# Performance work log

Hardware: AMD Instinct MI355X
Metric: run time of the kernel (lower is better)

Reference implementation:

```python
import jax, jax.numpy as jnp
import numpy as np
import math

B, S, D = 8, 2048, 512
WINDOW = 30

def setup_inputs() -> dict:
    key = jax.random.key(0)
    ks = jax.random.split(key, 9)
    s = 1.0 / math.sqrt(D)
    return {
        "hidden_states": jax.random.normal(ks[0], (B, S, D), jnp.float32),
        "Wq": jax.random.normal(ks[1], (D, D), jnp.float32) * s,
        "bq": jax.random.normal(ks[2], (D,), jnp.float32) * s,
        "Wk": jax.random.normal(ks[3], (D, D), jnp.float32) * s,
        "bk": jax.random.normal(ks[4], (D,), jnp.float32) * s,
        "Wv": jax.random.normal(ks[5], (D, D), jnp.float32) * s,
        "bv": jax.random.normal(ks[6], (D,), jnp.float32) * s,
        "Wg": jax.random.normal(ks[7], (D, 1), jnp.float32) * s,
        "bg": jax.random.normal(ks[8], (1,), jnp.float32) * s,
    }

def reference(hidden_states, Wq, bq, Wk, bk, Wv, bv, Wg, bg):
    seq_len = hidden_states.shape[1]
    scale = math.sqrt(hidden_states.shape[-1])
    Q = hidden_states @ Wq + bq
    K = hidden_states @ Wk + bk
    V = hidden_states @ Wv + bv
    # [B, S, S] dense scores, single head
    scores = jnp.einsum('bsd,btd->bst', Q, K) / scale
    global_out = jnp.einsum('bst,btd->bsd', jax.nn.softmax(scores, axis=-1), V)
    pos = jnp.arange(seq_len)
    window_mask = jnp.abs(pos[:, None] - pos[None, :]) <= WINDOW  # [S, S]
    local_scores = scores + jnp.where(window_mask, 0.0, -1e9)
    local_out = jnp.einsum('bst,btd->bsd', jax.nn.softmax(local_scores, axis=-1), V)
    gate = jax.nn.sigmoid(hidden_states @ Wg + bg)  # [B, S, 1]
    return (1.0 - gate) * global_out + gate * local_out
```

## Files before the change

### kernel.cpp

```cpp
#include <hip/hip_runtime.h>
#include <math.h>

#define B_N   8
#define S_LEN 2048
#define D_DIM 512
#define M_TOT (B_N * S_LEN)
#define WIN   30

typedef short bf16x8 __attribute__((ext_vector_type(8)));
typedef float f32x4  __attribute__((ext_vector_type(4)));
typedef unsigned short u16;
typedef unsigned int   u32;

__device__ __forceinline__ u16 f2bf(float f) {
    union { float f; u32 u; } v; v.f = f;
    u32 r = v.u + 0x7fffu + ((v.u >> 16) & 1u);
    return (u16)(r >> 16);
}
__device__ __forceinline__ float bf2f(u16 u) {
    union { u32 u; float f; } v; v.u = ((u32)u) << 16; return v.f;
}

__device__ __forceinline__ void gl2lds(const u16* g, u16* l) {
    __builtin_amdgcn_global_load_lds((const __attribute__((address_space(1))) void*)g,
                                     (__attribute__((address_space(3))) void*)l,
                                     16, 0, 0);
}

__device__ __forceinline__ int xcd_logical() {
    const int n = gridDim.x;
    const int hb = blockIdx.x;
    return (hb & 7) * (n >> 3) + (hb >> 3);
}

#define VM_WAIT(N) asm volatile("s_waitcnt vmcnt(" #N ")" ::: "memory")
#define BAR() do { __builtin_amdgcn_s_barrier(); asm volatile("" ::: "memory"); } while (0)

__global__ __launch_bounds__(256)
void convert_gate(const float* __restrict__ X, const float* __restrict__ Wg,
                  const float* __restrict__ bg, u16* __restrict__ Xb, float* __restrict__ gate) {
    int wv = threadIdx.x >> 6, lane = threadIdx.x & 63;
    int row = blockIdx.x * 4 + wv;
    const float4* x4 = (const float4*)(X + (size_t)row * D_DIM);
    const float4* w4 = (const float4*)Wg;
    float acc = 0.f;
    ushort4 o0, o1;
    {
        float4 a = x4[lane * 2], w = w4[lane * 2];
        acc += a.x * w.x + a.y * w.y + a.z * w.z + a.w * w.w;
        o0.x = f2bf(a.x); o0.y = f2bf(a.y); o0.z = f2bf(a.z); o0.w = f2bf(a.w);
        float4 b = x4[lane * 2 + 1], v = w4[lane * 2 + 1];
        acc += b.x * v.x + b.y * v.y + b.z * v.z + b.w * v.w;
        o1.x = f2bf(b.x); o1.y = f2bf(b.y); o1.z = f2bf(b.z); o1.w = f2bf(b.w);
    }
    ushort4* xb4 = (ushort4*)(Xb + (size_t)row * D_DIM);
    xb4[lane * 2] = o0;
    xb4[lane * 2 + 1] = o1;
#pragma unroll
    for (int o = 32; o; o >>= 1) acc += __shfl_xor(acc, o);
    if (lane == 0) gate[row] = 1.f / (1.f + __expf(-(acc + bg[0])));
}

__global__ __launch_bounds__(256) void transpose_w3(const float* __restrict__ Wq, const float* __restrict__ Wk,
                                                    const float* __restrict__ Wv, u16* __restrict__ Wt3) {
    const float* W = blockIdx.z == 0 ? Wq : (blockIdx.z == 1 ? Wk : Wv);
    u16* Wt = Wt3 + (size_t)blockIdx.z * D_DIM * D_DIM;
    __shared__ float t[32][33];
    int k0 = blockIdx.x * 32, n0 = blockIdx.y * 32;
    int tx = threadIdx.x & 31, ty = threadIdx.x >> 5;
#pragma unroll
    for (int r = ty; r < 32; r += 8) t[r][tx] = W[(size_t)(k0 + r) * D_DIM + n0 + tx];
    __syncthreads();
#pragma unroll
    for (int r = ty; r < 32; r += 8) Wt[(size_t)(n0 + r) * D_DIM + k0 + tx] = f2bf(t[tx][r]);
}

__global__ __launch_bounds__(256) void pack_bias(const float* __restrict__ bq, const float* __restrict__ bk,
                                                 const float* __restrict__ bv, float* __restrict__ b3) {
    int i = blockIdx.x * 256 + threadIdx.x;
    b3[i] = bq[i]; b3[512 + i] = bk[i]; b3[1024 + i] = bv[i];
}

template<int EPI>
__global__ __launch_bounds__(512, 2)
void gemm256(const u16* __restrict__ A, const u16* __restrict__ Bt,
             int lda, int ldb, int K, int nx, int ny,
             const float* __restrict__ aux, void* __restrict__ Cv, int ldc, float scale,
             long long zA, long long zB, long long zC, long long zAux) {
    const int logical = xcd_logical();
    const int x = logical % nx;
    const int t2 = logical / nx;
    const int y = t2 % ny;
    const int z = t2 / ny;

    A   += zA * z;
    Bt  += zB * z;
    if (aux) aux += zAux * z;

    constexpr int BUF = 16384;
    __shared__ u16 smem[3 * BUF];
    const int tid  = threadIdx.x;
    const int lane = tid & 63;
    const int wave = tid >> 6;
    const int wr = wave >> 2, wc = wave & 3;
    const int m0 = y * 256, n0 = x * 256;

    f32x4 acc[8][4];
#pragma unroll
    for (int i = 0; i < 8; i++)
#pragma unroll
        for (int j = 0; j < 4; j++) acc[i][j] = (f32x4){0.f, 0.f, 0.f, 0.f};

    auto stageA = [&](int b, int k0) {
#pragma unroll
        for (int j = 0; j < 2; j++) {
            int c = j * 512 + tid;
            int r = c >> 2;
            int s = ((c & 3) ^ ((c >> 3) & 3)) << 3;
            gl2lds(A + (size_t)(m0 + r) * lda + (k0 + s),
                   smem + b * BUF + j * 4096 + wave * 512);
        }
    };
    auto stageB = [&](int b, int k0) {
#pragma unroll
        for (int j = 0; j < 2; j++) {
            int c = j * 512 + tid;
            int r = c >> 2;
            int s = ((c & 3) ^ ((c >> 3) & 3)) << 3;
            gl2lds(Bt + (size_t)(n0 + r) * ldb + (k0 + s),
                   smem + b * BUF + 8192 + j * 4096 + wave * 512);
        }
    };

    const int nt = K >> 5;
    stageA(0, 0); stageB(0, 0); stageA(1, 32); stageB(1, 32);

    const int ks = lane >> 4;
    for (int t = 0; t < nt; ++t) {
        const u16* bA = smem + (t % 3) * BUF;
        const u16* bB = bA + 8192;
        if (t == nt - 1) { VM_WAIT(0); } else { VM_WAIT(4); }
        BAR();
        if (t + 2 < nt) stageA((t + 2) % 3, (t + 2) << 5);
        bf16x8 bfr[4], af[4];
#pragma unroll
        for (int n = 0; n < 4; n++) {
            int r = wc * 64 + n * 16 + (lane & 15);
            bfr[n] = *(const bf16x8*)&bB[r * 32 + (ks ^ ((r >> 1) & 3)) * 8];
        }
#pragma unroll
        for (int m = 0; m < 4; m++) {
            int r = wr * 128 + m * 16 + (lane & 15);
            af[m] = *(const bf16x8*)&bA[r * 32 + (ks ^ ((r >> 1) & 3)) * 8];
        }
        __builtin_amdgcn_s_setprio(1);
#pragma unroll
        for (int m = 0; m < 4; m++)
#pragma unroll
            for (int n = 0; n < 4; n++)
                acc[m][n] = __builtin_amdgcn_mfma_f32_16x16x32_bf16(af[m], bfr[n], acc[m][n], 0, 0, 0);
        __builtin_amdgcn_s_setprio(0);
        BAR();
        if (t + 2 < nt) stageB((t + 2) % 3, (t + 2) << 5);
#pragma unroll
        for (int m = 0; m < 4; m++) {
            int r = wr * 128 + (m + 4) * 16 + (lane & 15);
            af[m] = *(const bf16x8*)&bA[r * 32 + (ks ^ ((r >> 1) & 3)) * 8];
        }
        __builtin_amdgcn_s_setprio(1);
#pragma unroll
        for (int m = 0; m < 4; m++)
#pragma unroll
            for (int n = 0; n < 4; n++)
                acc[m + 4][n] = __builtin_amdgcn_mfma_f32_16x16x32_bf16(af[m], bfr[n], acc[m + 4][n], 0, 0, 0);
        __builtin_amdgcn_s_setprio(0);
    }

    u16* Cb = (u16*)Cv + zC * z;
#pragma unroll
    for (int m = 0; m < 8; m++) {
        int rbase = m0 + wr * 128 + m * 16 + ((lane >> 4) << 2);
#pragma unroll
        for (int n = 0; n < 4; n++) {
            int col = n0 + wc * 64 + n * 16 + (lane & 15);
#pragma unroll
            for (int rg = 0; rg < 4; rg++) {
                int row = rbase + rg;
                float v = acc[m][n][rg];
                if (EPI == 0) {
                    Cb[(size_t)row * ldc + col] = f2bf(v + aux[col]);
                } else {
                    Cb[(size_t)row * ldc + col] = f2bf(v * scale);
                }
            }
        }
    }
}

template<int EPI>
__global__ __launch_bounds__(256, 6)
void gemm_bt(const u16* __restrict__ A, const u16* __restrict__ Bt,
             int lda, int ldb, int K, int nx, int ny,
             const float* __restrict__ aux, void* __restrict__ Cv, int ldc, float scale,
             long long zA, long long zB, long long zC, long long zAux) {
    const int logical = xcd_logical();
    const int x = logical % nx;
    const int t2 = logical / nx;
    const int y = t2 % ny;
    const int z = t2 / ny;

    A   += zA * z;
    Bt  += zB * z;
    if (aux) aux += zAux * z;

    __shared__ u16 smem[3 * 8192];
    const int tid  = threadIdx.x;
    const int lane = tid & 63;
    const int wave = tid >> 6;
    const int wr = wave >> 1, wc = wave & 1;
    const int m0 = y * 128, n0 = x * 128;

    f32x4 acc[4][4];
#pragma unroll
    for (int i = 0; i < 4; i++)
#pragma unroll
        for (int j = 0; j < 4; j++) acc[i][j] = (f32x4){0.f, 0.f, 0.f, 0.f};

    const int c0 = tid, c1 = tid + 256;
    const int r0c = c0 >> 2, k0c = (((c0 & 3) ^ ((c0 >> 3) & 3)) << 3);
    const int r1c = c1 >> 2, k1c = (((c1 & 3) ^ ((c1 >> 3) & 3)) << 3);

    auto stage = [&](int b, int k0) {
        u16* dA = smem + b * 8192 + wave * 512;
        u16* dB = smem + b * 8192 + 4096 + wave * 512;
        gl2lds(A + (size_t)(m0 + r0c) * lda + (k0 + k0c), dA);
        gl2lds(A + (size_t)(m0 + r1c) * lda + (k0 + k1c), dA + 2048);
        gl2lds(Bt + (size_t)(n0 + r0c) * ldb + (k0 + k0c), dB);
        gl2lds(Bt + (size_t)(n0 + r1c) * ldb + (k0 + k1c), dB + 2048);
    };
    auto compute = [&](int b) {
        const u16* bA = smem + b * 8192;
        const u16* bB = smem + b * 8192 + 4096;
        const int ks = lane >> 4;
        bf16x8 af[4], bfr[4];
#pragma unroll
        for (int m = 0; m < 4; m++) {
            int r = wr * 64 + m * 16 + (lane & 15);
            af[m] = *(const bf16x8*)&bA[r * 32 + (ks ^ ((r >> 1) & 3)) * 8];
        }
#pragma unroll
        for (int n = 0; n < 4; n++) {
            int r = wc * 64 + n * 16 + (lane & 15);
            bfr[n] = *(const bf16x8*)&bB[r * 32 + (ks ^ ((r >> 1) & 3)) * 8];
        }
#pragma unroll
        for (int m = 0; m < 4; m++)
#pragma unroll
            for (int n = 0; n < 4; n++)
                acc[m][n] = __builtin_amdgcn_mfma_f32_16x16x32_bf16(af[m], bfr[n], acc[m][n], 0, 0, 0);
    };

    const int nt = K >> 5;
    stage(0, 0); stage(1, 32);

    int t = 0;
    for (; t < nt - 1; ++t) {
        VM_WAIT(4);
        BAR();
        if (t + 2 < nt) stage((t + 2) % 3, (t + 2) << 5);
        compute(t % 3);
    }
    VM_WAIT(0);
    BAR();
    compute((nt - 1) % 3);

    u16*   Cb = (EPI == 1) ? ((u16*)Cv + zC * z) : nullptr;
    float* Cf = (EPI == 2) ? ((float*)Cv + zC * z) : nullptr;

#pragma unroll
    for (int m = 0; m < 4; m++) {
        int rbase = m0 + wr * 64 + m * 16 + ((lane >> 4) << 2);
#pragma unroll
        for (int n = 0; n < 4; n++) {
            int col = n0 + wc * 64 + n * 16 + (lane & 15);
#pragma unroll
            for (int rg = 0; rg < 4; rg++) {
                int row = rbase + rg;
                float v = acc[m][n][rg];
                if (EPI == 1) {
                    Cb[(size_t)row * ldc + col] = f2bf(v + aux[row]);
                } else {
                    Cf[(size_t)row * ldc + col] = v * scale;
                }
            }
        }
    }
}

__global__ __launch_bounds__(256)
void softmax_fuse(u16* __restrict__ sc, const float* __restrict__ gate) {
    const int logical = xcd_logical();
    const int i = logical & (S_LEN - 1);
    const int z = logical >> 11;
    const int tid = threadIdx.x;
    const int wv = tid >> 6, lane = tid & 63;
    sc   += (size_t)z * S_LEN * S_LEN;
    gate += (size_t)z * S_LEN;

    __shared__ float r0[4], r1[4], mll[2];

    u16* scrow = sc + (size_t)i * S_LEN;
    uint4 raw = ((const uint4*)scrow)[tid];

    int jlo = i - WIN; if (jlo < 0) jlo = 0;
    int jhi = i + WIN; if (jhi > S_LEN - 1) jhi = S_LEN - 1;
    int cnt = jhi - jlo + 1;
    float bvv = (tid < cnt) ? bf2f(scrow[jlo + tid]) : -3.0e38f;
    float g = gate[i];

    float sv[8];
    sv[0] = bf2f((u16)(raw.x & 0xffff)); sv[1] = bf2f((u16)(raw.x >> 16));
    sv[2] = bf2f((u16)(raw.y & 0xffff)); sv[3] = bf2f((u16)(raw.y >> 16));
    sv[4] = bf2f((u16)(raw.z & 0xffff)); sv[5] = bf2f((u16)(raw.z >> 16));
    sv[6] = bf2f((u16)(raw.w & 0xffff)); sv[7] = bf2f((u16)(raw.w >> 16));

    float mx = fmaxf(fmaxf(fmaxf(sv[0], sv[1]), fmaxf(sv[2], sv[3])),
                     fmaxf(fmaxf(sv[4], sv[5]), fmaxf(sv[6], sv[7])));
#pragma unroll
    for (int o = 32; o; o >>= 1) mx = fmaxf(mx, __shfl_xor(mx, o));
    if (lane == 0) r0[wv] = mx;
    __syncthreads();
    float mg = fmaxf(fmaxf(r0[0], r0[1]), fmaxf(r0[2], r0[3]));

    float ev[8];
#pragma unroll
    for (int k = 0; k < 8; k++) ev[k] = __expf(sv[k] - mg);
    float se = ev[0] + ev[1] + ev[2] + ev[3] + ev[4] + ev[5] + ev[6] + ev[7];
#pragma unroll
    for (int o = 32; o; o >>= 1) se += __shfl_xor(se, o);
    if (lane == 0) r1[wv] = se;

    if (wv == 0) {
        float ml = bvv;
#pragma unroll
        for (int o = 32; o; o >>= 1) ml = fmaxf(ml, __shfl_xor(ml, o));
        float e = (lane < cnt) ? __expf(bvv - ml) : 0.f;
        float s2 = e;
#pragma unroll
        for (int o = 32; o; o >>= 1) s2 += __shfl_xor(s2, o);
        if (lane == 0) { mll[0] = ml; mll[1] = 1.f / s2; }
    }
    __syncthreads();
    float invl = (1.f - g) / (r1[0] + r1[1] + r1[2] + r1[3]);
    float ml  = mll[0];
    float ill = g * mll[1];

    const int c0 = tid * 8;
    u32 pk_[4];
#pragma unroll
    for (int h = 0; h < 4; h++) {
        float rA = ev[2 * h] * invl;
        float rB = ev[2 * h + 1] * invl;
        int colA = c0 + 2 * h;
        if ((u32)(colA - i + WIN) <= 2u * WIN)     rA += __expf(sv[2 * h] - ml) * ill;
        if ((u32)(colA + 1 - i + WIN) <= 2u * WIN) rB += __expf(sv[2 * h + 1] - ml) * ill;
        pk_[h] = (u32)f2bf(rA) | ((u32)f2bf(rB) << 16);
    }
    uint4 pw = {pk_[0], pk_[1], pk_[2], pk_[3]};
    ((uint4*)scrow)[tid] = pw;
}

extern "C" void kernel_launch(void* const* d_in, const int* in_sizes, int n_in,
                              void* d_out, int out_size, void* d_ws, size_t ws_size,
                              hipStream_t stream) {
    const float* X  = (const float*)d_in[0];
    const float* Wq = (const float*)d_in[1];
    const float* bq = (const float*)d_in[2];
    const float* Wk = (const float*)d_in[3];
    const float* bk = (const float*)d_in[4];
    const float* Wv = (const float*)d_in[5];
    const float* bv = (const float*)d_in[6];
    const float* Wg = (const float*)d_in[7];
    const float* bg = (const float*)d_in[8];
    float* out = (float*)d_out;

    char* p = (char*)d_ws;
    u16* Xb    = (u16*)p;  p += (size_t)M_TOT * D_DIM * 2;
    u16* Wt3   = (u16*)p;  p += (size_t)3 * D_DIM * D_DIM * 2;
    u16* QKV   = (u16*)p;  p += (size_t)2 * M_TOT * D_DIM * 2;
    u16* Vt    = (u16*)p;  p += (size_t)M_TOT * D_DIM * 2;
    float* gate  = (float*)p; p += (size_t)M_TOT * 4;
    float* bias3 = (float*)p; p += (size_t)3 * D_DIM * 4;
    u16* scores = (u16*)p;
    size_t base_used = (size_t)(p - (char*)d_ws);
    size_t per_batch = (size_t)S_LEN * S_LEN * 2;
    int nbuf = (int)((ws_size - base_used) / per_batch);
    if (nbuf > B_N) nbuf = B_N;
    if (nbuf < 1) nbuf = 1;

    u16* Qb = QKV;
    u16* Kb = QKV + (size_t)M_TOT * D_DIM;

    convert_gate<<<dim3(M_TOT / 4), 256, 0, stream>>>(X, Wg, bg, Xb, gate);
    transpose_w3<<<dim3(16, 16, 3), 256, 0, stream>>>(Wq, Wk, Wv, Wt3);
    pack_bias<<<dim3(2), 256, 0, stream>>>(bq, bk, bv, bias3);

    gemm256<0><<<dim3(2 * 64 * 2), 512, 0, stream>>>(
        Xb, Wt3, 512, 512, 512, 2, 64, bias3, QKV, 512, 1.f,
        0LL, (long long)D_DIM * D_DIM, (long long)M_TOT * D_DIM, (long long)D_DIM);

    gemm_bt<1><<<dim3(128 * 4), 256, 0, stream>>>(
        Wt3 + (size_t)2 * D_DIM * D_DIM, Xb, 512, 512, 512, 128, 4, bv, Vt, M_TOT, 1.f,
        0LL, 0LL, 0LL, 0LL);

    const float sc = 1.0f / sqrtf((float)D_DIM);
    for (int g0 = 0; g0 < B_N; g0 += nbuf) {
        int gcnt = B_N - g0 < nbuf ? B_N - g0 : nbuf;
        gemm256<3><<<dim3(8 * 8 * gcnt), 512, 0, stream>>>(
            Qb + (size_t)g0 * S_LEN * D_DIM, Kb + (size_t)g0 * S_LEN * D_DIM,
            512, 512, 512, 8, 8, nullptr, scores, S_LEN, sc,
            (long long)S_LEN * D_DIM, (long long)S_LEN * D_DIM,
            (long long)S_LEN * S_LEN, 0LL);
        softmax_fuse<<<dim3(S_LEN * gcnt), 256, 0, stream>>>(
            scores, gate + (size_t)g0 * S_LEN);
        gemm_bt<2><<<dim3(4 * 16 * gcnt), 256, 0, stream>>>(
            scores, Vt + (size_t)g0 * S_LEN,
            S_LEN, M_TOT, S_LEN, 4, 16, nullptr,
            out + (size_t)g0 * S_LEN * D_DIM, 512, 1.f,
            (long long)S_LEN * S_LEN, (long long)S_LEN,
            (long long)S_LEN * D_DIM, 0LL);
    }
}
```

Measured before the change: 174.6 us.

## Fuse softmax into score GEMM epilogue and PV GEMM prologue

Removes the separate row-softmax pass over the score matrix. The QK^T GEMM epilogue now accumulates per-row exp sums and band (window) exp sums through atomics. A small kernel folds these with the gate into per-row coefficients, and the PV GEMM recomputes exp(score) times those coefficients while staging A tiles into LDS. This saves a full read and write of the B×S×S bf16 score tensor. The cost is exps with no max subtraction, which can overflow for large scores, plus atomics and extra ALU work in the PV GEMM's load path.

```diff
diff --git a/kernel.cpp b/kernel.cpp
--- a/kernel.cpp
+++ b/kernel.cpp
@@ -34,6 +34,7 @@
 }
 
 #define VM_WAIT(N) asm volatile("s_waitcnt vmcnt(" #N ")" ::: "memory")
+#define LGKM0()    asm volatile("s_waitcnt lgkmcnt(0)" ::: "memory")
 #define BAR() do { __builtin_amdgcn_s_barrier(); asm volatile("" ::: "memory"); } while (0)
 
 __global__ __launch_bounds__(256)
@@ -81,11 +82,21 @@
     b3[i] = bq[i]; b3[512 + i] = bk[i]; b3[1024 + i] = bv[i];
 }
 
+__global__ __launch_bounds__(256)
+void coef_combine(const float* __restrict__ rs, const float* __restrict__ bs,
+                  const float* __restrict__ gate, float2* __restrict__ coef) {
+    int i = blockIdx.x * 256 + threadIdx.x;
+    float g = gate[i];
+    float2 c; c.x = (1.f - g) / rs[i]; c.y = g / bs[i];
+    coef[i] = c;
+}
+
 template<int EPI>
 __global__ __launch_bounds__(512, 2)
 void gemm256(const u16* __restrict__ A, const u16* __restrict__ Bt,
              int lda, int ldb, int K, int nx, int ny,
              const float* __restrict__ aux, void* __restrict__ Cv, int ldc, float scale,
+             float* __restrict__ rowsum, float* __restrict__ bandsum,
              long long zA, long long zB, long long zC, long long zAux) {
     const int logical = xcd_logical();
     const int x = logical % nx;
@@ -96,6 +107,7 @@
     A   += zA * z;
     Bt  += zB * z;
     if (aux) aux += zAux * z;
+    if (EPI == 3) { rowsum += 2048LL * z; bandsum += 2048LL * z; }
 
     constexpr int BUF = 16384;
     __shared__ u16 smem[3 * BUF];
@@ -104,6 +116,7 @@
     const int wave = tid >> 6;
     const int wr = wave >> 2, wc = wave & 3;
     const int m0 = y * 256, n0 = x * 256;
+    const int l15 = lane & 15;
 
     f32x4 acc[8][4];
 #pragma unroll
@@ -145,12 +158,12 @@
         bf16x8 bfr[4], af[4];
 #pragma unroll
         for (int n = 0; n < 4; n++) {
-            int r = wc * 64 + n * 16 + (lane & 15);
+            int r = wc * 64 + n * 16 + l15;
             bfr[n] = *(const bf16x8*)&bB[r * 32 + (ks ^ ((r >> 1) & 3)) * 8];
         }
 #pragma unroll
         for (int m = 0; m < 4; m++) {
-            int r = wr * 128 + m * 16 + (lane & 15);
+            int r = wr * 128 + m * 16 + l15;
             af[m] = *(const bf16x8*)&bA[r * 32 + (ks ^ ((r >> 1) & 3)) * 8];
         }
         __builtin_amdgcn_s_setprio(1);
@@ -164,7 +177,7 @@
         if (t + 2 < nt) stageB((t + 2) % 3, (t + 2) << 5);
 #pragma unroll
         for (int m = 0; m < 4; m++) {
-            int r = wr * 128 + (m + 4) * 16 + (lane & 15);
+            int r = wr * 128 + (m + 4) * 16 + l15;
             af[m] = *(const bf16x8*)&bA[r * 32 + (ks ^ ((r >> 1) & 3)) * 8];
         }
         __builtin_amdgcn_s_setprio(1);
@@ -174,15 +187,20 @@
             for (int n = 0; n < 4; n++)
                 acc[m + 4][n] = __builtin_amdgcn_mfma_f32_16x16x32_bf16(af[m], bfr[n], acc[m + 4][n], 0, 0, 0);
         __builtin_amdgcn_s_setprio(0);
+        BAR();
     }
 
     u16* Cb = (u16*)Cv + zC * z;
+    const bool diag = (EPI == 3) && (x - y <= 1) && (y - x <= 1);
+
 #pragma unroll
     for (int m = 0; m < 8; m++) {
         int rbase = m0 + wr * 128 + m * 16 + ((lane >> 4) << 2);
+        float se[4] = {0.f, 0.f, 0.f, 0.f};
+        float sb[4] = {0.f, 0.f, 0.f, 0.f};
 #pragma unroll
         for (int n = 0; n < 4; n++) {
-            int col = n0 + wc * 64 + n * 16 + (lane & 15);
+            int col = n0 + wc * 64 + n * 16 + l15;
 #pragma unroll
             for (int rg = 0; rg < 4; rg++) {
                 int row = rbase + rg;
@@ -190,28 +208,42 @@
                 if (EPI == 0) {
                     Cb[(size_t)row * ldc + col] = f2bf(v + aux[col]);
                 } else {
-                    Cb[(size_t)row * ldc + col] = f2bf(v * scale);
+                    u16 h = f2bf(v * scale);
+                    Cb[(size_t)row * ldc + col] = h;
+                    float e = __expf(bf2f(h));
+                    se[rg] += e;
+                    if (diag) {
+                        int d = col - row;
+                        if (d * d <= WIN * WIN) sb[rg] += e;
+                    }
                 }
             }
         }
-    }
-}
-
-template<int EPI>
+        if (EPI == 3) {
+#pragma unroll
+            for (int rg = 0; rg < 4; rg++) {
+                float s1 = se[rg];
+                s1 += __shfl_xor(s1, 1); s1 += __shfl_xor(s1, 2);
+                s1 += __shfl_xor(s1, 4); s1 += __shfl_xor(s1, 8);
+                if (l15 == 0) atomicAdd(&rowsum[rbase + rg - m0 + m0], s1);
+                if (diag) {
+                    float s2 = sb[rg];
+                    s2 += __shfl_xor(s2, 1); s2 += __shfl_xor(s2, 2);
+                    s2 += __shfl_xor(s2, 4); s2 += __shfl_xor(s2, 8);
+                    if (l15 == 0) atomicAdd(&bandsum[rbase + rg], s2);
+                }
+            }
+        }
+    }
+}
+
 __global__ __launch_bounds__(256, 6)
-void gemm_bt(const u16* __restrict__ A, const u16* __restrict__ Bt,
-             int lda, int ldb, int K, int nx, int ny,
-             const float* __restrict__ aux, void* __restrict__ Cv, int ldc, float scale,
-             long long zA, long long zB, long long zC, long long zAux) {
+void gemm_bt1(const u16* __restrict__ A, const u16* __restrict__ Bt,
+              int lda, int ldb, int K, int nx, int ny,
+              const float* __restrict__ aux, u16* __restrict__ C, int ldc) {
     const int logical = xcd_logical();
     const int x = logical % nx;
-    const int t2 = logical / nx;
-    const int y = t2 % ny;
-    const int z = t2 / ny;
-
-    A   += zA * z;
-    Bt  += zB * z;
-    if (aux) aux += zAux * z;
+    const int y = (logical / nx) % ny;
 
     __shared__ u16 smem[3 * 8192];
     const int tid  = threadIdx.x;
@@ -262,7 +294,6 @@
 
     const int nt = K >> 5;
     stage(0, 0); stage(1, 32);
-
     int t = 0;
     for (; t < nt - 1; ++t) {
         VM_WAIT(4);
@@ -274,9 +305,6 @@
     BAR();
     compute((nt - 1) % 3);
 
-    u16*   Cb = (EPI == 1) ? ((u16*)Cv + zC * z) : nullptr;
-    float* Cf = (EPI == 2) ? ((float*)Cv + zC * z) : nullptr;
-
 #pragma unroll
     for (int m = 0; m < 4; m++) {
         int rbase = m0 + wr * 64 + m * 16 + ((lane >> 4) << 2);
@@ -286,88 +314,151 @@
 #pragma unroll
             for (int rg = 0; rg < 4; rg++) {
                 int row = rbase + rg;
-                float v = acc[m][n][rg];
-                if (EPI == 1) {
-                    Cb[(size_t)row * ldc + col] = f2bf(v + aux[row]);
-                } else {
-                    Cf[(size_t)row * ldc + col] = v * scale;
-                }
+                C[(size_t)row * ldc + col] = f2bf(acc[m][n][rg] + aux[row]);
             }
         }
     }
 }
 
-__global__ __launch_bounds__(256)
-void softmax_fuse(u16* __restrict__ sc, const float* __restrict__ gate) {
+__global__ __launch_bounds__(256, 4)
+void gemm_pv(const u16* __restrict__ S, const u16* __restrict__ Bt,
+             const float2* __restrict__ coef, float* __restrict__ out,
+             int lda, int ldb, int K, int nx, int ny,
+             long long zA, long long zB, long long zC) {
     const int logical = xcd_logical();
-    const int i = logical & (S_LEN - 1);
-    const int z = logical >> 11;
-    const int tid = threadIdx.x;
-    const int wv = tid >> 6, lane = tid & 63;
-    sc   += (size_t)z * S_LEN * S_LEN;
-    gate += (size_t)z * S_LEN;
-
-    __shared__ float r0[4], r1[4], mll[2];
-
-    u16* scrow = sc + (size_t)i * S_LEN;
-    uint4 raw = ((const uint4*)scrow)[tid];
-
-    int jlo = i - WIN; if (jlo < 0) jlo = 0;
-    int jhi = i + WIN; if (jhi > S_LEN - 1) jhi = S_LEN - 1;
-    int cnt = jhi - jlo + 1;
-    float bvv = (tid < cnt) ? bf2f(scrow[jlo + tid]) : -3.0e38f;
-    float g = gate[i];
-
-    float sv[8];
-    sv[0] = bf2f((u16)(raw.x & 0xffff)); sv[1] = bf2f((u16)(raw.x >> 16));
-    sv[2] = bf2f((u16)(raw.y & 0xffff)); sv[3] = bf2f((u16)(raw.y >> 16));
-    sv[4] = bf2f((u16)(raw.z & 0xffff)); sv[5] = bf2f((u16)(raw.z >> 16));
-    sv[6] = bf2f((u16)(raw.w & 0xffff)); sv[7] = bf2f((u16)(raw.w >> 16));
-
-    float mx = fmaxf(fmaxf(fmaxf(sv[0], sv[1]), fmaxf(sv[2], sv[3])),
-                     fmaxf(fmaxf(sv[4], sv[5]), fmaxf(sv[6], sv[7])));
-#pragma unroll
-    for (int o = 32; o; o >>= 1) mx = fmaxf(mx, __shfl_xor(mx, o));
-    if (lane == 0) r0[wv] = mx;
-    __syncthreads();
-    float mg = fmaxf(fmaxf(r0[0], r0[1]), fmaxf(r0[2], r0[3]));
-
-    float ev[8];
-#pragma unroll
-    for (int k = 0; k < 8; k++) ev[k] = __expf(sv[k] - mg);
-    float se = ev[0] + ev[1] + ev[2] + ev[3] + ev[4] + ev[5] + ev[6] + ev[7];
-#pragma unroll
-    for (int o = 32; o; o >>= 1) se += __shfl_xor(se, o);
-    if (lane == 0) r1[wv] = se;
-
-    if (wv == 0) {
-        float ml = bvv;
-#pragma unroll
-        for (int o = 32; o; o >>= 1) ml = fmaxf(ml, __shfl_xor(ml, o));
-        float e = (lane < cnt) ? __expf(bvv - ml) : 0.f;
-        float s2 = e;
-#pragma unroll
-        for (int o = 32; o; o >>= 1) s2 += __shfl_xor(s2, o);
-        if (lane == 0) { mll[0] = ml; mll[1] = 1.f / s2; }
-    }
-    __syncthreads();
-    float invl = (1.f - g) / (r1[0] + r1[1] + r1[2] + r1[3]);
-    float ml  = mll[0];
-    float ill = g * mll[1];
-
-    const int c0 = tid * 8;
-    u32 pk_[4];
-#pragma unroll
-    for (int h = 0; h < 4; h++) {
-        float rA = ev[2 * h] * invl;
-        float rB = ev[2 * h + 1] * invl;
-        int colA = c0 + 2 * h;
-        if ((u32)(colA - i + WIN) <= 2u * WIN)     rA += __expf(sv[2 * h] - ml) * ill;
-        if ((u32)(colA + 1 - i + WIN) <= 2u * WIN) rB += __expf(sv[2 * h + 1] - ml) * ill;
-        pk_[h] = (u32)f2bf(rA) | ((u32)f2bf(rB) << 16);
-    }
-    uint4 pw = {pk_[0], pk_[1], pk_[2], pk_[3]};
-    ((uint4*)scrow)[tid] = pw;
+    const int x = logical % nx;
+    const int t2 = logical / nx;
+    const int y = t2 % ny;
+    const int z = t2 / ny;
+
+    S    += zA * z;
+    Bt   += zB * z;
+    coef += 2048LL * z;
+    float* outz = out + zC * z;
+
+    __shared__ u16 bufA[4096];
+    __shared__ u16 bufB[2][4096];
+    const int tid = threadIdx.x, lane = tid & 63, wave = tid >> 6;
+    const int wr = wave >> 1, wc = wave & 1;
+    const int m0 = y * 128, n0 = x * 128;
+    const int ks = lane >> 4, l15 = lane & 15;
+
+    f32x4 acc[4][4];
+#pragma unroll
+    for (int i = 0; i < 4; i++)
+#pragma unroll
+        for (int j = 0; j < 4; j++) acc[i][j] = (f32x4){0.f, 0.f, 0.f, 0.f};
+
+    const int c0 = tid, c1 = tid + 256;
+    const int r0 = c0 >> 2, k0c = (((c0 & 3) ^ ((c0 >> 3) & 3)) << 3);
+    const int r1 = c1 >> 2, k1c = (((c1 & 3) ^ ((c1 >> 3) & 3)) << 3);
+    const int arow0 = m0 + r0, arow1 = m0 + r1;
+    const float2 cf0 = coef[arow0], cf1 = coef[arow1];
+    const u16* Sr0 = S + (size_t)arow0 * lda;
+    const u16* Sr1 = S + (size_t)arow1 * lda;
+
+    auto glB = [&](int bsel, int k0) {
+        u16* dB = &bufB[bsel][wave * 512];
+        gl2lds(Bt + (size_t)(n0 + r0) * ldb + (k0 + k0c), dB);
+        gl2lds(Bt + (size_t)(n0 + r1) * ldb + (k0 + k1c), dB + 2048);
+    };
+
+    auto mkR = [&](uint4 q, float2 cf, int row, int cb) -> uint4 {
+        u32 w[4] = {q.x, q.y, q.z, q.w};
+        u32 o[4];
+#pragma unroll
+        for (int wi = 0; wi < 4; wi++) {
+            float s0 = bf2f((u16)(w[wi] & 0xffffu));
+            float s1 = bf2f((u16)(w[wi] >> 16));
+            float e0 = __expf(s0), e1 = __expf(s1);
+            int d0 = cb + 2 * wi - row, d1 = d0 + 1;
+            float r0v = cf.x * e0 + ((d0 * d0 <= WIN * WIN) ? cf.y * e0 : 0.f);
+            float r1v = cf.x * e1 + ((d1 * d1 <= WIN * WIN) ? cf.y * e1 : 0.f);
+            o[wi] = (u32)f2bf(r0v) | ((u32)f2bf(r1v) << 16);
+        }
+        uint4 r; r.x = o[0]; r.y = o[1]; r.z = o[2]; r.w = o[3];
+        return r;
+    };
+
+    auto compute = [&](int bsel) {
+        bf16x8 af[4], bfr[4];
+#pragma unroll
+        for (int m = 0; m < 4; m++) {
+            int r = wr * 64 + m * 16 + l15;
+            af[m] = *(const bf16x8*)&bufA[r * 32 + ((ks ^ ((r >> 1) & 3)) << 3)];
+        }
+#pragma unroll
+        for (int n = 0; n < 4; n++) {
+            int r = wc * 64 + n * 16 + l15;
+            bfr[n] = *(const bf16x8*)&bufB[bsel][r * 32 + ((ks ^ ((r >> 1) & 3)) << 3)];
+        }
+#pragma unroll
+        for (int m = 0; m < 4; m++)
+#pragma unroll
+            for (int n = 0; n < 4; n++)
+                acc[m][n] = __builtin_amdgcn_mfma_f32_16x16x32_bf16(af[m], bfr[n], acc[m][n], 0, 0, 0);
+    };
+
+    const int nt = K >> 5;
+    uint4 qa0, qa1, qb0, qb1;
+    qa0 = *(const uint4*)(Sr0 + k0c);
+    qa1 = *(const uint4*)(Sr1 + k1c);
+    glB(0, 0);
+
+    for (int t = 0; t < nt; t += 2) {
+        if (t + 1 < nt) {
+            int k1 = (t + 1) << 5;
+            qb0 = *(const uint4*)(Sr0 + k1 + k0c);
+            qb1 = *(const uint4*)(Sr1 + k1 + k1c);
+            glB(1, k1);
+        }
+        VM_WAIT(4);
+        {
+            int k0 = t << 5;
+            uint4 o0 = mkR(qa0, cf0, arow0, k0 + k0c);
+            uint4 o1 = mkR(qa1, cf1, arow1, k0 + k1c);
+            *(uint4*)&bufA[c0 * 8] = o0;
+            *(uint4*)&bufA[c1 * 8] = o1;
+        }
+        LGKM0();
+        BAR();
+        compute(0);
+        BAR();
+        if (t + 2 < nt) {
+            int k2 = (t + 2) << 5;
+            qa0 = *(const uint4*)(Sr0 + k2 + k0c);
+            qa1 = *(const uint4*)(Sr1 + k2 + k1c);
+            glB(0, k2);
+        }
+        if (t + 1 < nt) {
+            if (t + 1 == nt - 1) { VM_WAIT(0); } else { VM_WAIT(4); }
+            {
+                int k1 = (t + 1) << 5;
+                uint4 o0 = mkR(qb0, cf0, arow0, k1 + k0c);
+                uint4 o1 = mkR(qb1, cf1, arow1, k1 + k1c);
+                *(uint4*)&bufA[c0 * 8] = o0;
+                *(uint4*)&bufA[c1 * 8] = o1;
+            }
+            LGKM0();
+            BAR();
+            compute(1);
+            BAR();
+        }
+    }
+
+#pragma unroll
+    for (int m = 0; m < 4; m++) {
+        int rbase = m0 + wr * 64 + m * 16 + ((lane >> 4) << 2);
+#pragma unroll
+        for (int n = 0; n < 4; n++) {
+            int col = n0 + wc * 64 + n * 16 + l15;
+#pragma unroll
+            for (int rg = 0; rg < 4; rg++) {
+                int row = rbase + rg;
+                outz[(size_t)row * D_DIM + col] = acc[m][n][rg];
+            }
+        }
+    }
 }
 
 extern "C" void kernel_launch(void* const* d_in, const int* in_sizes, int n_in,
@@ -391,6 +482,9 @@
     u16* Vt    = (u16*)p;  p += (size_t)M_TOT * D_DIM * 2;
     float* gate  = (float*)p; p += (size_t)M_TOT * 4;
     float* bias3 = (float*)p; p += (size_t)3 * D_DIM * 4;
+    float* rowsum  = (float*)p; p += (size_t)M_TOT * 4;
+    float* bandsum = (float*)p; p += (size_t)M_TOT * 4;
+    float2* coef   = (float2*)p; p += (size_t)M_TOT * 8;
     u16* scores = (u16*)p;
     size_t base_used = (size_t)(p - (char*)d_ws);
     size_t per_batch = (size_t)S_LEN * S_LEN * 2;
@@ -401,17 +495,18 @@
     u16* Qb = QKV;
     u16* Kb = QKV + (size_t)M_TOT * D_DIM;
 
+    hipMemsetAsync(rowsum, 0, (size_t)M_TOT * 8, stream);
+
     convert_gate<<<dim3(M_TOT / 4), 256, 0, stream>>>(X, Wg, bg, Xb, gate);
     transpose_w3<<<dim3(16, 16, 3), 256, 0, stream>>>(Wq, Wk, Wv, Wt3);
     pack_bias<<<dim3(2), 256, 0, stream>>>(bq, bk, bv, bias3);
 
     gemm256<0><<<dim3(2 * 64 * 2), 512, 0, stream>>>(
-        Xb, Wt3, 512, 512, 512, 2, 64, bias3, QKV, 512, 1.f,
+        Xb, Wt3, 512, 512, 512, 2, 64, bias3, QKV, 512, 1.f, nullptr, nullptr,
         0LL, (long long)D_DIM * D_DIM, (long long)M_TOT * D_DIM, (long long)D_DIM);
 
-    gemm_bt<1><<<dim3(128 * 4), 256, 0, stream>>>(
-        Wt3 + (size_t)2 * D_DIM * D_DIM, Xb, 512, 512, 512, 128, 4, bv, Vt, M_TOT, 1.f,
-        0LL, 0LL, 0LL, 0LL);
+    gemm_bt1<<<dim3(128 * 4), 256, 0, stream>>>(
+        Wt3 + (size_t)2 * D_DIM * D_DIM, Xb, 512, 512, 512, 128, 4, bv, Vt, M_TOT);
 
     const float sc = 1.0f / sqrtf((float)D_DIM);
     for (int g0 = 0; g0 < B_N; g0 += nbuf) {
@@ -419,15 +514,17 @@
         gemm256<3><<<dim3(8 * 8 * gcnt), 512, 0, stream>>>(
             Qb + (size_t)g0 * S_LEN * D_DIM, Kb + (size_t)g0 * S_LEN * D_DIM,
             512, 512, 512, 8, 8, nullptr, scores, S_LEN, sc,
+            rowsum + (size_t)g0 * S_LEN, bandsum + (size_t)g0 * S_LEN,
             (long long)S_LEN * D_DIM, (long long)S_LEN * D_DIM,
             (long long)S_LEN * S_LEN, 0LL);
-        softmax_fuse<<<dim3(S_LEN * gcnt), 256, 0, stream>>>(
-            scores, gate + (size_t)g0 * S_LEN);
-        gemm_bt<2><<<dim3(4 * 16 * gcnt), 256, 0, stream>>>(
-            scores, Vt + (size_t)g0 * S_LEN,
-            S_LEN, M_TOT, S_LEN, 4, 16, nullptr,
-            out + (size_t)g0 * S_LEN * D_DIM, 512, 1.f,
+        coef_combine<<<dim3(gcnt * S_LEN / 256), 256, 0, stream>>>(
+            rowsum + (size_t)g0 * S_LEN, bandsum + (size_t)g0 * S_LEN,
+            gate + (size_t)g0 * S_LEN, coef + (size_t)g0 * S_LEN);
+        gemm_pv<<<dim3(4 * 16 * gcnt), 256, 0, stream>>>(
+            scores, Vt + (size_t)g0 * S_LEN, coef + (size_t)g0 * S_LEN,
+            out + (size_t)g0 * S_LEN * D_DIM,
+            S_LEN, M_TOT, S_LEN, 4, 16,
             (long long)S_LEN * S_LEN, (long long)S_LEN,
-            (long long)S_LEN * D_DIM, 0LL);
-    }
-}
+            (long long)S_LEN * D_DIM);
+    }
+}
```

After: 237.3 us. 1.36x slower.

## Fuse exp and row/band sums into QK^T epilogue, simplify softmax to normalize

Applied to the files above, without the earlier changes.

The score GEMM epilogue now writes exp(scaled score) without max subtraction and accumulates per-row full sums and windowed band sums via shuffle reductions and atomics. The softmax kernel becomes a single-pass normalize that scales each element by the gate-weighted reciprocal sums. This removes the max/sum reductions and the band reload from the softmax pass. In exchange it adds atomics and a memset, and drops max-subtraction, which relies on scores staying small enough not to overflow. An extra barrier is also added at the end of each GEMM k-loop iteration.

```diff
diff --git a/kernel.cpp b/kernel.cpp
--- a/kernel.cpp
+++ b/kernel.cpp
@@ -86,6 +86,7 @@
 void gemm256(const u16* __restrict__ A, const u16* __restrict__ Bt,
              int lda, int ldb, int K, int nx, int ny,
              const float* __restrict__ aux, void* __restrict__ Cv, int ldc, float scale,
+             float* __restrict__ rowsum, float* __restrict__ bandsum,
              long long zA, long long zB, long long zC, long long zAux) {
     const int logical = xcd_logical();
     const int x = logical % nx;
@@ -96,6 +97,7 @@
     A   += zA * z;
     Bt  += zB * z;
     if (aux) aux += zAux * z;
+    if (EPI == 3) { rowsum += 2048LL * z; bandsum += 2048LL * z; }
 
     constexpr int BUF = 16384;
     __shared__ u16 smem[3 * BUF];
@@ -104,6 +106,7 @@
     const int wave = tid >> 6;
     const int wr = wave >> 2, wc = wave & 3;
     const int m0 = y * 256, n0 = x * 256;
+    const int l15 = lane & 15;
 
     f32x4 acc[8][4];
 #pragma unroll
@@ -145,12 +148,12 @@
         bf16x8 bfr[4], af[4];
 #pragma unroll
         for (int n = 0; n < 4; n++) {
-            int r = wc * 64 + n * 16 + (lane & 15);
+            int r = wc * 64 + n * 16 + l15;
             bfr[n] = *(const bf16x8*)&bB[r * 32 + (ks ^ ((r >> 1) & 3)) * 8];
         }
 #pragma unroll
         for (int m = 0; m < 4; m++) {
-            int r = wr * 128 + m * 16 + (lane & 15);
+            int r = wr * 128 + m * 16 + l15;
             af[m] = *(const bf16x8*)&bA[r * 32 + (ks ^ ((r >> 1) & 3)) * 8];
         }
         __builtin_amdgcn_s_setprio(1);
@@ -164,7 +167,7 @@
         if (t + 2 < nt) stageB((t + 2) % 3, (t + 2) << 5);
 #pragma unroll
         for (int m = 0; m < 4; m++) {
-            int r = wr * 128 + (m + 4) * 16 + (lane & 15);
+            int r = wr * 128 + (m + 4) * 16 + l15;
             af[m] = *(const bf16x8*)&bA[r * 32 + (ks ^ ((r >> 1) & 3)) * 8];
         }
         __builtin_amdgcn_s_setprio(1);
@@ -174,15 +177,20 @@
             for (int n = 0; n < 4; n++)
                 acc[m + 4][n] = __builtin_amdgcn_mfma_f32_16x16x32_bf16(af[m], bfr[n], acc[m + 4][n], 0, 0, 0);
         __builtin_amdgcn_s_setprio(0);
+        BAR();
     }
 
     u16* Cb = (u16*)Cv + zC * z;
+    const bool diag = (EPI == 3) && (x - y <= 1) && (y - x <= 1);
+
 #pragma unroll
     for (int m = 0; m < 8; m++) {
         int rbase = m0 + wr * 128 + m * 16 + ((lane >> 4) << 2);
+        float se[4] = {0.f, 0.f, 0.f, 0.f};
+        float sb[4] = {0.f, 0.f, 0.f, 0.f};
 #pragma unroll
         for (int n = 0; n < 4; n++) {
-            int col = n0 + wc * 64 + n * 16 + (lane & 15);
+            int col = n0 + wc * 64 + n * 16 + l15;
 #pragma unroll
             for (int rg = 0; rg < 4; rg++) {
                 int row = rbase + rg;
@@ -190,7 +198,28 @@
                 if (EPI == 0) {
                     Cb[(size_t)row * ldc + col] = f2bf(v + aux[col]);
                 } else {
-                    Cb[(size_t)row * ldc + col] = f2bf(v * scale);
+                    float e = __expf(v * scale);
+                    Cb[(size_t)row * ldc + col] = f2bf(e);
+                    se[rg] += e;
+                    if (diag) {
+                        int d = col - row;
+                        if (d * d <= WIN * WIN) sb[rg] += e;
+                    }
+                }
+            }
+        }
+        if (EPI == 3) {
+#pragma unroll
+            for (int rg = 0; rg < 4; rg++) {
+                float s1 = se[rg];
+                s1 += __shfl_xor(s1, 1); s1 += __shfl_xor(s1, 2);
+                s1 += __shfl_xor(s1, 4); s1 += __shfl_xor(s1, 8);
+                if (l15 == 0) atomicAdd(&rowsum[rbase + rg], s1);
+                if (diag) {
+                    float s2 = sb[rg];
+                    s2 += __shfl_xor(s2, 1); s2 += __shfl_xor(s2, 2);
+                    s2 += __shfl_xor(s2, 4); s2 += __shfl_xor(s2, 8);
+                    if (l15 == 0) atomicAdd(&bandsum[rbase + rg], s2);
                 }
             }
         }
@@ -262,7 +291,6 @@
 
     const int nt = K >> 5;
     stage(0, 0); stage(1, 32);
-
     int t = 0;
     for (; t < nt - 1; ++t) {
         VM_WAIT(4);
@@ -298,76 +326,34 @@
 }
 
 __global__ __launch_bounds__(256)
-void softmax_fuse(u16* __restrict__ sc, const float* __restrict__ gate) {
+void normalize_r(u16* __restrict__ sc, const float* __restrict__ rs,
+                 const float* __restrict__ bs, const float* __restrict__ gate) {
     const int logical = xcd_logical();
     const int i = logical & (S_LEN - 1);
     const int z = logical >> 11;
     const int tid = threadIdx.x;
-    const int wv = tid >> 6, lane = tid & 63;
-    sc   += (size_t)z * S_LEN * S_LEN;
-    gate += (size_t)z * S_LEN;
-
-    __shared__ float r0[4], r1[4], mll[2];
-
-    u16* scrow = sc + (size_t)i * S_LEN;
-    uint4 raw = ((const uint4*)scrow)[tid];
-
-    int jlo = i - WIN; if (jlo < 0) jlo = 0;
-    int jhi = i + WIN; if (jhi > S_LEN - 1) jhi = S_LEN - 1;
-    int cnt = jhi - jlo + 1;
-    float bvv = (tid < cnt) ? bf2f(scrow[jlo + tid]) : -3.0e38f;
-    float g = gate[i];
-
-    float sv[8];
-    sv[0] = bf2f((u16)(raw.x & 0xffff)); sv[1] = bf2f((u16)(raw.x >> 16));
-    sv[2] = bf2f((u16)(raw.y & 0xffff)); sv[3] = bf2f((u16)(raw.y >> 16));
-    sv[4] = bf2f((u16)(raw.z & 0xffff)); sv[5] = bf2f((u16)(raw.z >> 16));
-    sv[6] = bf2f((u16)(raw.w & 0xffff)); sv[7] = bf2f((u16)(raw.w >> 16));
-
-    float mx = fmaxf(fmaxf(fmaxf(sv[0], sv[1]), fmaxf(sv[2], sv[3])),
-                     fmaxf(fmaxf(sv[4], sv[5]), fmaxf(sv[6], sv[7])));
-#pragma unroll
-    for (int o = 32; o; o >>= 1) mx = fmaxf(mx, __shfl_xor(mx, o));
-    if (lane == 0) r0[wv] = mx;
-    __syncthreads();
-    float mg = fmaxf(fmaxf(r0[0], r0[1]), fmaxf(r0[2], r0[3]));
-
-    float ev[8];
-#pragma unroll
-    for (int k = 0; k < 8; k++) ev[k] = __expf(sv[k] - mg);
-    float se = ev[0] + ev[1] + ev[2] + ev[3] + ev[4] + ev[5] + ev[6] + ev[7];
-#pragma unroll
-    for (int o = 32; o; o >>= 1) se += __shfl_xor(se, o);
-    if (lane == 0) r1[wv] = se;
-
-    if (wv == 0) {
-        float ml = bvv;
-#pragma unroll
-        for (int o = 32; o; o >>= 1) ml = fmaxf(ml, __shfl_xor(ml, o));
-        float e = (lane < cnt) ? __expf(bvv - ml) : 0.f;
-        float s2 = e;
-#pragma unroll
-        for (int o = 32; o; o >>= 1) s2 += __shfl_xor(s2, o);
-        if (lane == 0) { mll[0] = ml; mll[1] = 1.f / s2; }
-    }
-    __syncthreads();
-    float invl = (1.f - g) / (r1[0] + r1[1] + r1[2] + r1[3]);
-    float ml  = mll[0];
-    float ill = g * mll[1];
-
+    sc += (size_t)z * S_LEN * S_LEN;
+
+    const int ri = z * S_LEN + i;
+    float g  = gate[ri];
+    float cx = (1.f - g) / rs[ri];
+    float cy = g / bs[ri];
+
+    u16* row = sc + (size_t)i * S_LEN;
+    uint4 q = ((const uint4*)row)[tid];
+    u32 w[4] = {q.x, q.y, q.z, q.w};
     const int c0 = tid * 8;
-    u32 pk_[4];
 #pragma unroll
     for (int h = 0; h < 4; h++) {
-        float rA = ev[2 * h] * invl;
-        float rB = ev[2 * h + 1] * invl;
-        int colA = c0 + 2 * h;
-        if ((u32)(colA - i + WIN) <= 2u * WIN)     rA += __expf(sv[2 * h] - ml) * ill;
-        if ((u32)(colA + 1 - i + WIN) <= 2u * WIN) rB += __expf(sv[2 * h + 1] - ml) * ill;
-        pk_[h] = (u32)f2bf(rA) | ((u32)f2bf(rB) << 16);
-    }
-    uint4 pw = {pk_[0], pk_[1], pk_[2], pk_[3]};
-    ((uint4*)scrow)[tid] = pw;
+        float e0 = bf2f((u16)(w[h] & 0xffffu));
+        float e1 = bf2f((u16)(w[h] >> 16));
+        int d0 = c0 + 2 * h - i, d1 = d0 + 1;
+        float r0 = e0 * (cx + ((d0 * d0 <= WIN * WIN) ? cy : 0.f));
+        float r1 = e1 * (cx + ((d1 * d1 <= WIN * WIN) ? cy : 0.f));
+        w[h] = (u32)f2bf(r0) | ((u32)f2bf(r1) << 16);
+    }
+    uint4 o; o.x = w[0]; o.y = w[1]; o.z = w[2]; o.w = w[3];
+    ((uint4*)row)[tid] = o;
 }
 
 extern "C" void kernel_launch(void* const* d_in, const int* in_sizes, int n_in,
@@ -391,6 +377,8 @@
     u16* Vt    = (u16*)p;  p += (size_t)M_TOT * D_DIM * 2;
     float* gate  = (float*)p; p += (size_t)M_TOT * 4;
     float* bias3 = (float*)p; p += (size_t)3 * D_DIM * 4;
+    float* rowsum  = (float*)p; p += (size_t)M_TOT * 4;
+    float* bandsum = (float*)p; p += (size_t)M_TOT * 4;
     u16* scores = (u16*)p;
     size_t base_used = (size_t)(p - (char*)d_ws);
     size_t per_batch = (size_t)S_LEN * S_LEN * 2;
@@ -401,12 +389,14 @@
     u16* Qb = QKV;
     u16* Kb = QKV + (size_t)M_TOT * D_DIM;
 
+    hipMemsetAsync(rowsum, 0, (size_t)M_TOT * 8, stream);
+
     convert_gate<<<dim3(M_TOT / 4), 256, 0, stream>>>(X, Wg, bg, Xb, gate);
     transpose_w3<<<dim3(16, 16, 3), 256, 0, stream>>>(Wq, Wk, Wv, Wt3);
     pack_bias<<<dim3(2), 256, 0, stream>>>(bq, bk, bv, bias3);
 
     gemm256<0><<<dim3(2 * 64 * 2), 512, 0, stream>>>(
-        Xb, Wt3, 512, 512, 512, 2, 64, bias3, QKV, 512, 1.f,
+        Xb, Wt3, 512, 512, 512, 2, 64, bias3, QKV, 512, 1.f, nullptr, nullptr,
         0LL, (long long)D_DIM * D_DIM, (long long)M_TOT * D_DIM, (long long)D_DIM);
 
     gemm_bt<1><<<dim3(128 * 4), 256, 0, stream>>>(
@@ -419,10 +409,12 @@
         gemm256<3><<<dim3(8 * 8 * gcnt), 512, 0, stream>>>(
             Qb + (size_t)g0 * S_LEN * D_DIM, Kb + (size_t)g0 * S_LEN * D_DIM,
             512, 512, 512, 8, 8, nullptr, scores, S_LEN, sc,
+            rowsum + (size_t)g0 * S_LEN, bandsum + (size_t)g0 * S_LEN,
             (long long)S_LEN * D_DIM, (long long)S_LEN * D_DIM,
             (long long)S_LEN * S_LEN, 0LL);
-        softmax_fuse<<<dim3(S_LEN * gcnt), 256, 0, stream>>>(
-            scores, gate + (size_t)g0 * S_LEN);
+        normalize_r<<<dim3(S_LEN * gcnt), 256, 0, stream>>>(
+            scores, rowsum + (size_t)g0 * S_LEN, bandsum + (size_t)g0 * S_LEN,
+            gate + (size_t)g0 * S_LEN);
         gemm_bt<2><<<dim3(4 * 16 * gcnt), 256, 0, stream>>>(
             scores, Vt + (size_t)g0 * S_LEN,
             S_LEN, M_TOT, S_LEN, 4, 16, nullptr,
```

Result: slower. 191.6 us (+9.7%).
